# Kernel optimization log

Measured on AMD Instinct MI355X. Metric: run time of the kernel, lower is better.

## Reference

```python
import jax, jax.numpy as jnp
import numpy as np

PATCH = 3  # patch_size=3, stride=1
B, C, H, W = 8, 256, 64, 64


def _extract_patches(x):
    # x: (c, h, w) -> (c*PATCH*PATCH, N) with N = (h-2)*(w-2), valid 3x3 patches
    c, h, w = x.shape
    hh, ww = h - PATCH + 1, w - PATCH + 1
    pats = jnp.stack([x[:, i:i + hh, j:j + ww]
                      for i in range(PATCH) for j in range(PATCH)], axis=0)  # (9, c, hh, ww)
    return pats.reshape(PATCH * PATCH * c, hh * ww)


def _index_to_flow(max_idx):
    # max_idx: (hh, ww) int -> flow (h, w, 2) padded by 2 at bottom/right
    hh, ww = max_idx.shape
    flow_w = (max_idx % ww).astype(jnp.float32)
    flow_h = (max_idx // ww).astype(jnp.float32)
    gy, gx = jnp.meshgrid(jnp.arange(hh, dtype=jnp.float32),
                          jnp.arange(ww, dtype=jnp.float32), indexing='ij')
    flow = jnp.stack((flow_w - gx, flow_h - gy), axis=2)  # (hh, ww, 2)
    return jnp.pad(flow, ((0, 2), (0, 2), (0, 0)))


def _per_image(feat_in, feat_ref):
    c, h, w = feat_in.shape
    hh, ww = h - PATCH + 1, w - PATCH + 1
    # channel-wise L2 normalize each spatial position (F.normalize dim=0, eps=1e-12)
    feat_in = feat_in / jnp.maximum(jnp.linalg.norm(feat_in, axis=0, keepdims=True), 1e-12)
    feat_ref = feat_ref / jnp.maximum(jnp.linalg.norm(feat_ref, axis=0, keepdims=True), 1e-12)
    Pi = _extract_patches(feat_in)    # (k, N)
    Pr = _extract_patches(feat_ref)   # (k, N)
    # is_norm=True: normalize ref patches (norm + 1e-5, per BasicSR feature_match_index)
    Pr = Pr / (jnp.linalg.norm(Pr, axis=0, keepdims=True) + 1e-5)
    corr = Pi.T @ Pr                  # (N, N) exhaustive patch correlation
    max_val = corr.max(axis=1)
    max_idx = jnp.argmax(corr, axis=1)
    # norm_input=True: divide by input patch norms
    max_val = max_val / jnp.linalg.norm(Pi, axis=0)
    max_val = max_val.reshape(hh, ww)
    max_idx = max_idx.reshape(hh, ww)
    sim = jnp.pad(max_val, ((1, 1), (1, 1)))[None]  # (1, h, w)
    flow = _index_to_flow(max_idx)                   # (h, w, 2)
    # nine down-right shifts (fill 0 at top-left), tensor_shift semantics
    shifted = jnp.stack([jnp.pad(flow[:h - i, :w - j], ((i, 0), (j, 0), (0, 0)))
                         for i in range(3) for j in range(3)], axis=0)  # (9, h, w, 2)
    return flow, shifted, sim


def setup_inputs() -> dict:
    key = jax.random.key(0)
    k1, k2 = jax.random.split(key)
    features1 = jax.random.normal(k1, (B, C, H, W), dtype=jnp.float32)
    features2 = jax.random.normal(k2, (B, C, H, W), dtype=jnp.float32)
    return {"features1": features1, "features2": features2}


def reference(features1, features2):
    pre_flow, pre_offset, pre_similarity = jax.vmap(_per_image)(features1, features2)
    # pre_flow: (b,h,w,2); pre_offset: (b,9,h,w,2); pre_similarity: (b,1,h,w)
    return pre_flow, pre_offset, pre_similarity
```

## Files before the change

### kernel.cpp

```cpp
#include <hip/hip_runtime.h>

typedef unsigned short u16;
typedef unsigned char u8;
typedef unsigned int u32;
typedef __bf16 bf16x8 __attribute__((ext_vector_type(8)));
typedef float f32x4 __attribute__((ext_vector_type(4)));

constexpr int BATCH = 8;
constexpr int C = 256;
constexpr int H = 64;
constexpr int W = 64;
constexpr int HW = H * W;
constexpr int HH = 62, WW = 62;
constexpr int NQ = HH * WW;
constexpr int SEG = 8;
constexpr int NBLK_RED = 536;

constexpr size_t OFF_RNORM = 0;
constexpr size_t OFF_RESV = 262144;
constexpr size_t OFF_RESI = 385280;
constexpr size_t OFF_PV = 508416;
constexpr size_t OFF_PI = OFF_PV + 62980096;
constexpr size_t OFF_SLOT0 = OFF_PI + 15745024;
constexpr size_t SP_H1 = 0;
constexpr size_t SP_L1 = 2097152;
constexpr size_t SP_H2 = 4194304;
constexpr size_t SP_L2 = 6291456;
constexpr size_t SP_Q = 8388608;
constexpr size_t SLOT_BYTES = 75513856;
constexpr size_t PVIMG = (size_t)NQ * 512;

typedef const __attribute__((address_space(1))) unsigned int* gas_ptr;
typedef __attribute__((address_space(3))) unsigned int* las_ptr;
__device__ __forceinline__ void gl16(const void* g, void* l) {
  __builtin_amdgcn_global_load_lds((gas_ptr)g, (las_ptr)l, 16, 0, 0);
}

__device__ __forceinline__ int pre_of(int ki) {
  if (ki <= 62) return ki * (ki + 1) / 2;
  int r = 123 - ki;
  return 1953 + 1891 - r * (r + 1) / 2;
}

__global__ __launch_bounds__(256) void norm_kernel(const float* __restrict__ f1,
                                                   const float* __restrict__ f2,
                                                   float* __restrict__ rnorm) {
  int by = blockIdx.x;
  int tensor = blockIdx.y;
  const float* f = tensor ? f2 : f1;
  int b = by >> 6, y = by & 63;
  int x = threadIdx.x & 63;
  int cq = threadIdx.x >> 6;
  const float* base = f + ((size_t)b * C) * HW + y * W + x;
  float s = 0.f;
  for (int c = cq; c < C; c += 4) {
    float v = base[(size_t)c * HW];
    s = fmaf(v, v, s);
  }
  __shared__ float sm[4][64];
  sm[cq][x] = s;
  __syncthreads();
  if (threadIdx.x < 64) {
    float t = sm[0][x] + sm[1][x] + sm[2][x] + sm[3][x];
    float nrm = fmaxf(sqrtf(t), 1e-12f);
    rnorm[((size_t)tensor * BATCH + b) * HW + y * W + x] = 1.0f / nrm;
  }
}

__device__ __forceinline__ void convert_body(int chunk, int tensor, int bi,
                                             const float* __restrict__ f1,
                                             const float* __restrict__ f2,
                                             const float* __restrict__ rnorm,
                                             char* slot, char* smemraw, int t) {
  typedef u32 row_t[257];
  row_t* sm = (row_t*)smemraw;
  int pos0 = chunk * 32;
  const float* f = (tensor ? f2 : f1) + (size_t)bi * C * HW;
  const float* rn = rnorm + ((size_t)tensor * BATCH + bi) * HW + pos0;
  u16* dh = (u16*)(slot + (tensor ? SP_H2 : SP_H1)) + (size_t)pos0 * C;
  u16* dl = (u16*)(slot + (tensor ? SP_L2 : SP_L1)) + (size_t)pos0 * C;

  int px = t & 31, cg = t >> 5;
  float r = rn[px];
  for (int kk = 0; kk < 32; ++kk) {
    int c = (cg << 5) + kk;
    float v = f[(size_t)c * HW + pos0 + px] * r;
    __bf16 h = (__bf16)v;
    float hf = (float)h;
    __bf16 lo = (__bf16)(v - hf);
    sm[px][c] = ((u32)__builtin_bit_cast(u16, h) << 16) | (u32)__builtin_bit_cast(u16, lo);
  }
  __syncthreads();
  int px2 = t >> 3, seg = t & 7;
  int c0 = seg * 32;
  for (int g8 = 0; g8 < 4; ++g8) {
    u32 hw0, hw1, hw2, hw3, lw0, lw1, lw2, lw3;
    u32 a, b2;
    a = sm[px2][c0 + g8 * 8 + 0]; b2 = sm[px2][c0 + g8 * 8 + 1];
    hw0 = (a >> 16) | (b2 & 0xFFFF0000u); lw0 = (a & 0xFFFFu) | (b2 << 16);
    a = sm[px2][c0 + g8 * 8 + 2]; b2 = sm[px2][c0 + g8 * 8 + 3];
    hw1 = (a >> 16) | (b2 & 0xFFFF0000u); lw1 = (a & 0xFFFFu) | (b2 << 16);
    a = sm[px2][c0 + g8 * 8 + 4]; b2 = sm[px2][c0 + g8 * 8 + 5];
    hw2 = (a >> 16) | (b2 & 0xFFFF0000u); lw2 = (a & 0xFFFFu) | (b2 << 16);
    a = sm[px2][c0 + g8 * 8 + 6]; b2 = sm[px2][c0 + g8 * 8 + 7];
    hw3 = (a >> 16) | (b2 & 0xFFFF0000u); lw3 = (a & 0xFFFFu) | (b2 << 16);
    size_t off = (size_t)px2 * C + c0 + g8 * 8;
    uint4 hv; hv.x = hw0; hv.y = hw1; hv.z = hw2; hv.w = hw3;
    uint4 lv; lv.x = lw0; lv.y = lw1; lv.z = lw2; lv.w = lw3;
    *(uint4*)(dh + off) = hv;
    *(uint4*)(dl + off) = lv;
  }
}

__device__ __forceinline__ void pgemm_body(int bid, char* slot, char* smem, int t) {
  const u16* hi1 = (const u16*)(slot + SP_H1);
  const u16* lo1 = (const u16*)(slot + SP_L1);
  const u16* hi2 = (const u16*)(slot + SP_H2);
  const u16* lo2 = (const u16*)(slot + SP_L2);
  float* P = (float*)(slot + SP_Q);

  int xcd = bid & 7, idx = bid >> 3;
  int p0 = (((xcd >> 1) * 8 + (idx >> 4)) << 7);
  int q0 = (((xcd & 1) * 16 + (idx & 15)) << 7);

  int l = t & 63, w = t >> 6, wm = w >> 1, wn = w & 1;
  int lr = l & 15, lh = l >> 4;

  const u16* srcs[4] = {hi1 + (size_t)p0 * 256, lo1 + (size_t)p0 * 256,
                        hi2 + (size_t)q0 * 256, lo2 + (size_t)q0 * 256};

  f32x4 acc[4][4];
#pragma unroll
  for (int mf = 0; mf < 4; ++mf)
#pragma unroll
    for (int nf = 0; nf < 4; ++nf)
      acc[mf][nf] = (f32x4){0.f, 0.f, 0.f, 0.f};

  auto stage = [&](int b, int kt) {
    char* base = smem + b * 32768;
#pragma unroll
    for (int pl = 0; pl < 4; ++pl) {
      const u16* s = srcs[pl];
#pragma unroll
      for (int wq = 0; wq < 2; ++wq) {
        int ci = (w * 2 + wq) * 64 + l;
        int row = ci >> 2, sl = ci & 3;
        int q = sl ^ ((row >> 1) & 3);
        size_t goff = (size_t)row * 256 + kt * 32 + (q << 3);
        gl16(s + goff, base + pl * 8192 + (w * 2 + wq) * 1024 + l * 16);
      }
    }
  };

  stage(0, 0);
  stage(1, 1);
  asm volatile("s_waitcnt vmcnt(8)" ::: "memory");
  __builtin_amdgcn_sched_barrier(0);
  __builtin_amdgcn_s_barrier();
  __builtin_amdgcn_sched_barrier(0);

#pragma unroll
  for (int kt = 0; kt < 8; ++kt) {
    int b = kt & 1;
    char* sAh = smem + b * 32768;
    char* sAl = sAh + 8192;
    char* sBh = sAh + 16384;
    char* sBl = sAh + 24576;
    bf16x8 ah[4], al[4];
#pragma unroll
    for (int mf = 0; mf < 4; ++mf) {
      int row = wm * 64 + mf * 16 + lr;
      int off = row * 64 + ((lh ^ ((row >> 1) & 3)) << 4);
      ah[mf] = *(const bf16x8*)(sAh + off);
      al[mf] = *(const bf16x8*)(sAl + off);
    }
#pragma unroll
    for (int nf = 0; nf < 4; ++nf) {
      int row = wn * 64 + nf * 16 + lr;
      int off = row * 64 + ((lh ^ ((row >> 1) & 3)) << 4);
      bf16x8 bh = *(const bf16x8*)(sBh + off);
      bf16x8 bl = *(const bf16x8*)(sBl + off);
#pragma unroll
      for (int mf = 0; mf < 4; ++mf) {
        acc[mf][nf] = __builtin_amdgcn_mfma_f32_16x16x32_bf16(ah[mf], bh, acc[mf][nf], 0, 0, 0);
        acc[mf][nf] = __builtin_amdgcn_mfma_f32_16x16x32_bf16(al[mf], bh, acc[mf][nf], 0, 0, 0);
        acc[mf][nf] = __builtin_amdgcn_mfma_f32_16x16x32_bf16(ah[mf], bl, acc[mf][nf], 0, 0, 0);
      }
    }
    if (kt == 7) break;
    __builtin_amdgcn_sched_barrier(0);
    __builtin_amdgcn_s_barrier();
    __builtin_amdgcn_sched_barrier(0);
    if (kt < 6) {
      stage(b, kt + 2);
      asm volatile("s_waitcnt vmcnt(8)" ::: "memory");
    } else {
      asm volatile("s_waitcnt vmcnt(0)" ::: "memory");
    }
    __builtin_amdgcn_sched_barrier(0);
    __builtin_amdgcn_s_barrier();
    __builtin_amdgcn_sched_barrier(0);
  }
  __syncthreads();

  float* sq = (float*)smem;
#pragma unroll
  for (int pass = 0; pass < 2; ++pass) {
    if (pass) __syncthreads();
    if (wn == pass) {
      float* buf = sq + wm * 4352;
#pragma unroll
      for (int mf = 0; mf < 4; ++mf)
#pragma unroll
        for (int nf = 0; nf < 4; ++nf)
#pragma unroll
          for (int j = 0; j < 4; ++j)
            buf[(mf * 16 + lh * 4 + j) * 68 + nf * 16 + lr] = acc[mf][nf][j];
      *(f32x4*)(buf + l * 68 + 64) = (f32x4){0.f, 0.f, 0.f, 0.f};
    }
    __syncthreads();
    int tid2 = t & 127, sel = t >> 7;
    int ax = tid2 & 63, halfj = tid2 >> 6;
    const float* S = sq + sel * 4352;
    int rr1 = ax + 1 > 63 ? 63 : ax + 1;
    int rr2 = ax + 2 > 63 ? 63 : ax + 2;
    const float* S0 = S + ax * 68;
    const float* S1 = S + rr1 * 68;
    const float* S2 = S + rr2 * 68;
    int planeIdx = (((p0 >> 6) + sel) << 6) + (q0 >> 6) + pass;
    float* Qp = P + (((size_t)planeIdx) << 12);
#pragma unroll
    for (int gi = 0; gi < 4; ++gi) {
      int g = halfj * 4 + gi;
      int c0 = g * 8;
      float r0[12], r1a[12], r2a[12];
#pragma unroll
      for (int u = 0; u < 3; ++u) {
        *(f32x4*)(r0 + u * 4) = *(const f32x4*)(S0 + c0 + u * 4);
        *(f32x4*)(r1a + u * 4) = *(const f32x4*)(S1 + c0 + u * 4);
        *(f32x4*)(r2a + u * 4) = *(const f32x4*)(S2 + c0 + u * 4);
      }
      f32x4 qv0, qv1;
#pragma unroll
      for (int e = 0; e < 4; ++e) qv0[e] = r0[e] + r1a[e + 1] + r2a[e + 2];
#pragma unroll
      for (int e = 0; e < 4; ++e) qv1[e] = r0[e + 4] + r1a[e + 5] + r2a[e + 6];
      float* Qg = Qp + g * 512 + (ax << 2);
      __builtin_nontemporal_store(qv0, (f32x4*)(Qg));
      __builtin_nontemporal_store(qv1, (f32x4*)(Qg + 256));
    }
  }
}

__device__ __forceinline__ void reduce_body(int rid, const char* slot,
                                            float* pval8, u8* pidx8, int t) {
  const float* QT = (const float*)(slot + SP_Q);

  int bid = rid;
  int ki = 0;
  for (ki = 0; ki < 123; ++ki) {
    int d = ki - 61; if (d < 0) d = -d;
    int ns = (62 - d + SEG - 1) / SEG;
    if (bid < ns) break;
    bid -= ns;
  }
  int k = ki - 61;
  int ystart = k < 0 ? -k : 0;
  int yend = k > 0 ? 61 - k : 61;
  int y0 = ystart + bid * SEG;
  int y1 = y0 + SEG; if (y1 > yend + 1) y1 = yend + 1;
  int sid0 = pre_of(ki) + (y0 - ystart);
  int pmax = yend + 2;

  int w2 = t >> 6, l = t & 63;

  float A[16], B[16], P0[16], P1[16], P2[16];

  auto ld = [&](int p, float* D) {
    const float* gp = QT + (((size_t)((p << 6) + (p + k))) << 12) + (l << 2);
#pragma unroll
    for (int h = 0; h < 2; ++h) {
      const float* g2 = gp + ((w2 + h * 4) << 9);
      *(f32x4*)(D + h * 8) = __builtin_nontemporal_load((const f32x4*)g2);
      *(f32x4*)(D + h * 8 + 4) = __builtin_nontemporal_load((const f32x4*)(g2 + 256));
    }
  };

  auto candstep = [&](int y, const float* D0, const float* D1, const float* D2) {
#pragma unroll
    for (int h = 0; h < 2; ++h) {
      int ww = w2 + h * 4;
      float best = __uint_as_float(0xFF800000u);
      int bbb = 0;
#pragma unroll
      for (int s = 0; s < 8; ++s) {
        float c = D0[h * 8 + s] + D1[h * 8 + s] + D2[h * 8 + s];
        bool valid = (ww * 8 + s) <= 61;
        if (valid && c > best) { best = c; bbb = s; }
      }
      size_t o = (size_t)(sid0 + (y - y0)) * 512 + (ww << 6) + l;
      pval8[o] = best;
      pidx8[o] = (u8)bbb;
    }
  };

  ld(y0, A);
  ld(y0 + 1, B);
  ld(y0 + 2, P0);
  ld(y0 + 3 > pmax ? pmax : y0 + 3, P1);
  ld(y0 + 4 > pmax ? pmax : y0 + 4, P2);

  int y = y0;
  while (true) {
    candstep(y, A, B, P0);
#pragma unroll
    for (int s = 0; s < 16; ++s) { A[s] = B[s]; B[s] = P0[s]; }
    if (++y >= y1) break;
    ld(y + 4 > pmax ? pmax : y + 4, P0);
    candstep(y, A, B, P1);
#pragma unroll
    for (int s = 0; s < 16; ++s) { A[s] = B[s]; B[s] = P1[s]; }
    if (++y >= y1) break;
    ld(y + 4 > pmax ? pmax : y + 4, P1);
    candstep(y, A, B, P2);
#pragma unroll
    for (int s = 0; s < 16; ++s) { A[s] = B[s]; B[s] = P2[s]; }
    if (++y >= y1) break;
    ld(y + 4 > pmax ? pmax : y + 4, P2);
  }
}

__global__ __launch_bounds__(256) void convert_kernel(const float* __restrict__ f1,
                                                      const float* __restrict__ f2,
                                                      const float* __restrict__ rnorm,
                                                      int bi, char* __restrict__ slot) {
  __shared__ __align__(16) char smem[33024];
  convert_body(blockIdx.x, blockIdx.y, bi, f1, f2, rnorm, slot, smem, threadIdx.x);
}

__global__ __launch_bounds__(256, 2) void merged_kernel(const float* __restrict__ f1,
                                                        const float* __restrict__ f2,
                                                        const float* __restrict__ rnorm,
                                                        char* __restrict__ ws,
                                                        int pg_img, int rd_img, int cv_img) {
  __shared__ __align__(16) char smem[65536];
  int bx = blockIdx.x, t = threadIdx.x;
  char* slot0 = ws + OFF_SLOT0;

  if (bx < 1608) {
    int m = bx % 3;
    if (m < 2) {
      int pid = (bx / 3) * 2 + m;
      if (pg_img >= 0 && pid < 1024)
        pgemm_body(pid, slot0 + (size_t)(pg_img & 1) * SLOT_BYTES, smem, t);
    } else {
      int rid = bx / 3;
      if (rd_img >= 0) {
        float* pv = (float*)(ws + OFF_PV) + (size_t)rd_img * PVIMG;
        u8* pi = (u8*)(ws + OFF_PI) + (size_t)rd_img * PVIMG;
        reduce_body(rid, slot0 + (size_t)(rd_img & 1) * SLOT_BYTES, pv, pi, t);
      }
    }
  } else {
    int cid = bx - 1608;
    if (cv_img >= 0)
      convert_body(cid & 127, cid >> 7, cv_img, f1, f2, rnorm,
                   slot0 + (size_t)(cv_img & 1) * SLOT_BYTES, smem, t);
  }
}

__global__ __launch_bounds__(256) void combine_kernel(const char* __restrict__ ws,
                                                      float* __restrict__ resv,
                                                      int* __restrict__ residx) {
  int q = blockIdx.x * 256 + threadIdx.x;
  if (q >= NQ) return;
  int b = blockIdx.y;
  const float* pval8 = (const float*)(ws + OFF_PV) + (size_t)b * PVIMG;
  const u8* pidx8 = (const u8*)(ws + OFF_PI) + (size_t)b * PVIMG;
  int y = q / 62, ax = q - y * 62;
  float best = __uint_as_float(0xFF800000u);
  int bjy = 0, bw = 0;
  for (int jy = 0; jy < 62; ++jy) {
    int ki = 61 + jy - y;
    int sid = pre_of(ki) + (y < jy ? y : jy);
    const float* p = pval8 + (size_t)sid * 512 + ax;
#pragma unroll
    for (int ww = 0; ww < 8; ++ww) {
      float v = p[ww << 6];
      if (v > best) { best = v; bjy = jy; bw = ww; }
    }
  }
  int kib = 61 + bjy - y;
  int sidb = pre_of(kib) + (y < bjy ? y : bjy);
  int bb = pidx8[(size_t)sidb * 512 + (bw << 6) + ax];
  resv[(size_t)b * NQ + q] = best;
  residx[(size_t)b * NQ + q] = bjy * 62 + bw * 8 + bb;
}

__global__ __launch_bounds__(256) void assemble_kernel(const float* __restrict__ res_val,
                                                       const int* __restrict__ res_idx,
                                                       float* __restrict__ out) {
  int gid = blockIdx.x * 256 + threadIdx.x;
  if (gid >= BATCH * HW) return;
  int b = gid >> 12;
  int y = (gid >> 6) & 63;
  int x = gid & 63;

  float* out_flow = out;
  float* out_off = out + (size_t)BATCH * HW * 2;
  float* out_sim = out + (size_t)BATCH * HW * 2 + (size_t)BATCH * 9 * HW * 2;

  auto flow_at = [&](int yy, int xx, float* fx, float* fy) {
    if (yy >= 0 && yy < HH && xx >= 0 && xx < WW) {
      int idx = res_idx[(size_t)b * NQ + yy * WW + xx];
      *fx = (float)(idx % WW - xx);
      *fy = (float)(idx / WW - yy);
    } else {
      *fx = 0.f;
      *fy = 0.f;
    }
  };

  float fx, fy;
  flow_at(y, x, &fx, &fy);
  size_t fo = ((size_t)b * HW + y * W + x) * 2;
  out_flow[fo + 0] = fx;
  out_flow[fo + 1] = fy;

#pragma unroll
  for (int sft = 0; sft < 9; ++sft) {
    int i = sft / 3, jj = sft % 3;
    float ox, oy;
    flow_at(y - i, x - jj, &ox, &oy);
    size_t o = (((size_t)b * 9 + sft) * HW + y * W + x) * 2;
    out_off[o + 0] = ox;
    out_off[o + 1] = oy;
  }

  float sim = 0.f;
  if (y >= 1 && y <= HH && x >= 1 && x <= WW) {
    float mv = res_val[(size_t)b * NQ + (y - 1) * WW + (x - 1)];
    sim = mv * (1.0f / ((3.0f + 1e-5f) * 3.0f));
  }
  out_sim[(size_t)b * HW + y * W + x] = sim;
}

extern "C" void kernel_launch(void* const* d_in, const int* in_sizes, int n_in,
                              void* d_out, int out_size, void* d_ws, size_t ws_size,
                              hipStream_t stream) {
  const float* f1 = (const float*)d_in[0];
  const float* f2 = (const float*)d_in[1];
  float* out = (float*)d_out;
  char* ws = (char*)d_ws;

  float* rnorm = (float*)(ws + OFF_RNORM);
  float* resv = (float*)(ws + OFF_RESV);
  int* residx = (int*)(ws + OFF_RESI);
  char* slot0 = ws + OFF_SLOT0;

  norm_kernel<<<dim3(BATCH * H, 2), 256, 0, stream>>>(f1, f2, rnorm);
  convert_kernel<<<dim3(128, 2), 256, 0, stream>>>(f1, f2, rnorm, 0, slot0);

  for (int i = 0; i < 8; ++i) {
    int cv = (i + 1 < 8) ? i + 1 : -1;
    merged_kernel<<<1864, 256, 0, stream>>>(f1, f2, rnorm, ws, i, i - 1, cv);
  }
  merged_kernel<<<1864, 256, 0, stream>>>(f1, f2, rnorm, ws, -1, 7, -1);

  combine_kernel<<<dim3(16, BATCH), 256, 0, stream>>>(ws, resv, residx);

  int total = BATCH * HW;
  assemble_kernel<<<(total + 255) / 256, 256, 0, stream>>>(resv, residx, out);
}
```

Baseline: 467.1 us.

## Double block size to 512 threads, halving per-thread work in all phases

Blocks of the merged and convert kernels grow from 256 to 512 threads. Each thread now does half the work: the GEMM tile is split across 8 waves with a 4x2 fragment accumulator, staging is one load per plane, and the reduction and convert loops are halved. The aim is more waves in flight and lower register pressure, to hide latency better. The cost is more LDS contention per block and a tighter 512x4 launch-bound register budget.

```diff
diff --git a/kernel.cpp b/kernel.cpp
--- a/kernel.cpp
+++ b/kernel.cpp
@@ -82,8 +82,8 @@
 
   int px = t & 31, cg = t >> 5;
   float r = rn[px];
-  for (int kk = 0; kk < 32; ++kk) {
-    int c = (cg << 5) + kk;
+  for (int kk = 0; kk < 16; ++kk) {
+    int c = (cg << 4) + kk;
     float v = f[(size_t)c * HW + pos0 + px] * r;
     __bf16 h = (__bf16)v;
     float hf = (float)h;
@@ -91,9 +91,9 @@
     sm[px][c] = ((u32)__builtin_bit_cast(u16, h) << 16) | (u32)__builtin_bit_cast(u16, lo);
   }
   __syncthreads();
-  int px2 = t >> 3, seg = t & 7;
-  int c0 = seg * 32;
-  for (int g8 = 0; g8 < 4; ++g8) {
+  int px2 = t >> 4, seg = t & 15;
+  int c0 = seg * 16;
+  for (int g8 = 0; g8 < 2; ++g8) {
     u32 hw0, hw1, hw2, hw3, lw0, lw1, lw2, lw3;
     u32 a, b2;
     a = sm[px2][c0 + g8 * 8 + 0]; b2 = sm[px2][c0 + g8 * 8 + 1];
@@ -123,38 +123,33 @@
   int p0 = (((xcd >> 1) * 8 + (idx >> 4)) << 7);
   int q0 = (((xcd & 1) * 16 + (idx & 15)) << 7);
 
-  int l = t & 63, w = t >> 6, wm = w >> 1, wn = w & 1;
+  int l = t & 63, w = t >> 6;
+  int wm = w & 1, wq4 = w >> 1;
   int lr = l & 15, lh = l >> 4;
 
   const u16* srcs[4] = {hi1 + (size_t)p0 * 256, lo1 + (size_t)p0 * 256,
                         hi2 + (size_t)q0 * 256, lo2 + (size_t)q0 * 256};
 
-  f32x4 acc[4][4];
+  f32x4 acc[4][2];
 #pragma unroll
   for (int mf = 0; mf < 4; ++mf)
 #pragma unroll
-    for (int nf = 0; nf < 4; ++nf)
+    for (int nf = 0; nf < 2; ++nf)
       acc[mf][nf] = (f32x4){0.f, 0.f, 0.f, 0.f};
 
   auto stage = [&](int b, int kt) {
     char* base = smem + b * 32768;
-#pragma unroll
-    for (int pl = 0; pl < 4; ++pl) {
-      const u16* s = srcs[pl];
-#pragma unroll
-      for (int wq = 0; wq < 2; ++wq) {
-        int ci = (w * 2 + wq) * 64 + l;
-        int row = ci >> 2, sl = ci & 3;
-        int q = sl ^ ((row >> 1) & 3);
-        size_t goff = (size_t)row * 256 + kt * 32 + (q << 3);
-        gl16(s + goff, base + pl * 8192 + (w * 2 + wq) * 1024 + l * 16);
-      }
-    }
+    int row = t >> 2, sl = t & 3;
+    int q = sl ^ ((row >> 1) & 3);
+    size_t goff = (size_t)row * 256 + kt * 32 + (q << 3);
+#pragma unroll
+    for (int pl = 0; pl < 4; ++pl)
+      gl16(srcs[pl] + goff, base + pl * 8192 + t * 16);
   };
 
   stage(0, 0);
   stage(1, 1);
-  asm volatile("s_waitcnt vmcnt(8)" ::: "memory");
+  asm volatile("s_waitcnt vmcnt(4)" ::: "memory");
   __builtin_amdgcn_sched_barrier(0);
   __builtin_amdgcn_s_barrier();
   __builtin_amdgcn_sched_barrier(0);
@@ -175,8 +170,8 @@
       al[mf] = *(const bf16x8*)(sAl + off);
     }
 #pragma unroll
-    for (int nf = 0; nf < 4; ++nf) {
-      int row = wn * 64 + nf * 16 + lr;
+    for (int nf = 0; nf < 2; ++nf) {
+      int row = wq4 * 32 + nf * 16 + lr;
       int off = row * 64 + ((lh ^ ((row >> 1) & 3)) << 4);
       bf16x8 bh = *(const bf16x8*)(sBh + off);
       bf16x8 bl = *(const bf16x8*)(sBl + off);
@@ -193,7 +188,7 @@
     __builtin_amdgcn_sched_barrier(0);
     if (kt < 6) {
       stage(b, kt + 2);
-      asm volatile("s_waitcnt vmcnt(8)" ::: "memory");
+      asm volatile("s_waitcnt vmcnt(4)" ::: "memory");
     } else {
       asm volatile("s_waitcnt vmcnt(0)" ::: "memory");
     }
@@ -207,31 +202,33 @@
 #pragma unroll
   for (int pass = 0; pass < 2; ++pass) {
     if (pass) __syncthreads();
-    if (wn == pass) {
+    if ((wq4 >> 1) == pass) {
       float* buf = sq + wm * 4352;
+      int cbase = (wq4 & 1) * 32;
 #pragma unroll
       for (int mf = 0; mf < 4; ++mf)
 #pragma unroll
-        for (int nf = 0; nf < 4; ++nf)
+        for (int nf = 0; nf < 2; ++nf)
 #pragma unroll
           for (int j = 0; j < 4; ++j)
-            buf[(mf * 16 + lh * 4 + j) * 68 + nf * 16 + lr] = acc[mf][nf][j];
-      *(f32x4*)(buf + l * 68 + 64) = (f32x4){0.f, 0.f, 0.f, 0.f};
+            buf[(mf * 16 + lh * 4 + j) * 68 + cbase + nf * 16 + lr] = acc[mf][nf][j];
+      if ((wq4 & 1) == 0)
+        *(f32x4*)(buf + l * 68 + 64) = (f32x4){0.f, 0.f, 0.f, 0.f};
     }
     __syncthreads();
-    int tid2 = t & 127, sel = t >> 7;
-    int ax = tid2 & 63, halfj = tid2 >> 6;
-    const float* S = sq + sel * 4352;
+    int sel = t >> 8, rest = t & 255;
+    int ax = rest & 63, quarter = rest >> 6;
     int rr1 = ax + 1 > 63 ? 63 : ax + 1;
     int rr2 = ax + 2 > 63 ? 63 : ax + 2;
+    const float* S = sq + sel * 4352;
     const float* S0 = S + ax * 68;
     const float* S1 = S + rr1 * 68;
     const float* S2 = S + rr2 * 68;
     int planeIdx = (((p0 >> 6) + sel) << 6) + (q0 >> 6) + pass;
     float* Qp = P + (((size_t)planeIdx) << 12);
 #pragma unroll
-    for (int gi = 0; gi < 4; ++gi) {
-      int g = halfj * 4 + gi;
+    for (int gi2 = 0; gi2 < 2; ++gi2) {
+      int g = quarter * 2 + gi2;
       int c0 = g * 8;
       float r0[12], r1a[12], r2a[12];
 #pragma unroll
@@ -274,34 +271,26 @@
 
   int w2 = t >> 6, l = t & 63;
 
-  float A[16], B[16], P0[16], P1[16], P2[16];
+  float A[8], B[8], P0[8], P1[8], P2[8];
 
   auto ld = [&](int p, float* D) {
-    const float* gp = QT + (((size_t)((p << 6) + (p + k))) << 12) + (l << 2);
-#pragma unroll
-    for (int h = 0; h < 2; ++h) {
-      const float* g2 = gp + ((w2 + h * 4) << 9);
-      *(f32x4*)(D + h * 8) = __builtin_nontemporal_load((const f32x4*)g2);
-      *(f32x4*)(D + h * 8 + 4) = __builtin_nontemporal_load((const f32x4*)(g2 + 256));
-    }
+    const float* gp = QT + (((size_t)((p << 6) + (p + k))) << 12) + (w2 << 9) + (l << 2);
+    *(f32x4*)(D) = __builtin_nontemporal_load((const f32x4*)gp);
+    *(f32x4*)(D + 4) = __builtin_nontemporal_load((const f32x4*)(gp + 256));
   };
 
   auto candstep = [&](int y, const float* D0, const float* D1, const float* D2) {
-#pragma unroll
-    for (int h = 0; h < 2; ++h) {
-      int ww = w2 + h * 4;
-      float best = __uint_as_float(0xFF800000u);
-      int bbb = 0;
-#pragma unroll
-      for (int s = 0; s < 8; ++s) {
-        float c = D0[h * 8 + s] + D1[h * 8 + s] + D2[h * 8 + s];
-        bool valid = (ww * 8 + s) <= 61;
-        if (valid && c > best) { best = c; bbb = s; }
-      }
-      size_t o = (size_t)(sid0 + (y - y0)) * 512 + (ww << 6) + l;
-      pval8[o] = best;
-      pidx8[o] = (u8)bbb;
-    }
+    float best = __uint_as_float(0xFF800000u);
+    int bbb = 0;
+#pragma unroll
+    for (int s = 0; s < 8; ++s) {
+      float c = D0[s] + D1[s] + D2[s];
+      bool valid = (w2 * 8 + s) <= 61;
+      if (valid && c > best) { best = c; bbb = s; }
+    }
+    size_t o = (size_t)(sid0 + (y - y0)) * 512 + (w2 << 6) + l;
+    pval8[o] = best;
+    pidx8[o] = (u8)bbb;
   };
 
   ld(y0, A);
@@ -314,23 +303,23 @@
   while (true) {
     candstep(y, A, B, P0);
 #pragma unroll
-    for (int s = 0; s < 16; ++s) { A[s] = B[s]; B[s] = P0[s]; }
+    for (int s = 0; s < 8; ++s) { A[s] = B[s]; B[s] = P0[s]; }
     if (++y >= y1) break;
     ld(y + 4 > pmax ? pmax : y + 4, P0);
     candstep(y, A, B, P1);
 #pragma unroll
-    for (int s = 0; s < 16; ++s) { A[s] = B[s]; B[s] = P1[s]; }
+    for (int s = 0; s < 8; ++s) { A[s] = B[s]; B[s] = P1[s]; }
     if (++y >= y1) break;
     ld(y + 4 > pmax ? pmax : y + 4, P1);
     candstep(y, A, B, P2);
 #pragma unroll
-    for (int s = 0; s < 16; ++s) { A[s] = B[s]; B[s] = P2[s]; }
+    for (int s = 0; s < 8; ++s) { A[s] = B[s]; B[s] = P2[s]; }
     if (++y >= y1) break;
     ld(y + 4 > pmax ? pmax : y + 4, P2);
   }
 }
 
-__global__ __launch_bounds__(256) void convert_kernel(const float* __restrict__ f1,
+__global__ __launch_bounds__(512) void convert_kernel(const float* __restrict__ f1,
                                                       const float* __restrict__ f2,
                                                       const float* __restrict__ rnorm,
                                                       int bi, char* __restrict__ slot) {
@@ -338,7 +327,7 @@
   convert_body(blockIdx.x, blockIdx.y, bi, f1, f2, rnorm, slot, smem, threadIdx.x);
 }
 
-__global__ __launch_bounds__(256, 2) void merged_kernel(const float* __restrict__ f1,
+__global__ __launch_bounds__(512, 4) void merged_kernel(const float* __restrict__ f1,
                                                         const float* __restrict__ f2,
                                                         const float* __restrict__ rnorm,
                                                         char* __restrict__ ws,
@@ -459,13 +448,13 @@
   char* slot0 = ws + OFF_SLOT0;
 
   norm_kernel<<<dim3(BATCH * H, 2), 256, 0, stream>>>(f1, f2, rnorm);
-  convert_kernel<<<dim3(128, 2), 256, 0, stream>>>(f1, f2, rnorm, 0, slot0);
+  convert_kernel<<<dim3(128, 2), 512, 0, stream>>>(f1, f2, rnorm, 0, slot0);
 
   for (int i = 0; i < 8; ++i) {
     int cv = (i + 1 < 8) ? i + 1 : -1;
-    merged_kernel<<<1864, 256, 0, stream>>>(f1, f2, rnorm, ws, i, i - 1, cv);
-  }
-  merged_kernel<<<1864, 256, 0, stream>>>(f1, f2, rnorm, ws, -1, 7, -1);
+    merged_kernel<<<1864, 512, 0, stream>>>(f1, f2, rnorm, ws, i, i - 1, cv);
+  }
+  merged_kernel<<<1864, 512, 0, stream>>>(f1, f2, rnorm, ws, -1, 7, -1);
 
   combine_kernel<<<dim3(16, BATCH), 256, 0, stream>>>(ws, resv, residx);
 
```

After: 452.1 us (median of 2 runs). 3.2% less time.
